# Optimization experiments

Measured on AMD Instinct MI355X. Metric: run time of the kernel, lower is better.

Reference implementation:

```python
import jax, jax.numpy as jnp
import numpy as np

jax.config.update("jax_enable_x64", True)  # faithful int64 hash arithmetic

N2_SIZES = [6619, 6637, 6653, 6659, 6661, 6673, 6679, 6689]
N3_SIZES = [65521, 65537, 65539, 65543, 65551, 65557, 65563, 65579]
SLOT_DIM = 80  # 1280 / (2 orders * 8 heads)
NUM_HEADS = 8
BATCH, SEQ = 8, 4096
VOCAB = 50257


def setup_inputs() -> dict:
    key = jax.random.key(0)
    ks = jax.random.split(key, 2 + 16)
    inp = {
        "canonical_ids": jax.random.randint(ks[0], (BATCH, SEQ), 0, VOCAB, dtype=jnp.int64),
        "hash_seeds": jax.random.randint(ks[1], (3, NUM_HEADS), 1, 2**31 - 1, dtype=jnp.int64),
    }
    i = 2
    for n, sizes in ((2, N2_SIZES), (3, N3_SIZES)):
        for h, sz in enumerate(sizes):
            inp[f"w_n{n}_h{h}"] = 0.02 * jax.random.normal(ks[i], (sz, SLOT_DIM), dtype=jnp.float32)
            i += 1
    return inp


def _ngrams(ids, n):
    # suffix n-grams per position, left-padded with 0: [B, S, n]
    padded = jnp.pad(ids, ((0, 0), (n - 1, 0)))
    S = ids.shape[1]
    return jnp.stack([padded[:, i:i + S] for i in range(n)], axis=-1)


def reference(canonical_ids, hash_seeds,
              w_n2_h0, w_n2_h1, w_n2_h2, w_n2_h3, w_n2_h4, w_n2_h5, w_n2_h6, w_n2_h7,
              w_n3_h0, w_n3_h1, w_n3_h2, w_n3_h3, w_n3_h4, w_n3_h5, w_n3_h6, w_n3_h7):
    tables = {
        2: [w_n2_h0, w_n2_h1, w_n2_h2, w_n2_h3, w_n2_h4, w_n2_h5, w_n2_h6, w_n2_h7],
        3: [w_n3_h0, w_n3_h1, w_n3_h2, w_n3_h3, w_n3_h4, w_n3_h5, w_n3_h6, w_n3_h7],
    }
    sizes = {2: N2_SIZES, 3: N3_SIZES}
    outs = []
    for n in (2, 3):
        ng = _ngrams(canonical_ids, n)                              # [B, S, n] int64
        seeds = hash_seeds[:n].T                                    # [H, n]
        terms = ng[:, :, None, :] * seeds[None, None, :, :]         # [B, S, H, n]
        h = terms[..., 0]
        for i in range(1, n):
            h = h ^ terms[..., i]                                   # [B, S, H]
        for k in range(NUM_HEADS):
            idx = h[:, :, k] % sizes[n][k]                          # [B, S]
            outs.append(tables[n][k][idx])                          # [B, S, SLOT_DIM]
    return jnp.concatenate(outs, axis=-1)                           # [B, S, 1280]
```

## Files before the change

### kernel.cpp

```cpp
#include <hip/hip_runtime.h>

typedef unsigned long long ull;
typedef float f4 __attribute__((ext_vector_type(4)));

__constant__ unsigned kSizes[16] = {
    6619u, 6637u, 6653u, 6659u, 6661u, 6673u, 6679u, 6689u,
    65521u, 65537u, 65539u, 65543u, 65551u, 65557u, 65563u, 65579u
};

__global__ __launch_bounds__(256)
void engram_idx_kernel(const int* __restrict__ ids,
                       const int* __restrict__ seeds,
                       int* __restrict__ idx_out)
{
    const int tid  = blockIdx.x * 256 + threadIdx.x;
    const int pos  = tid >> 4;
    const int slot = tid & 15;
    const int b = pos >> 12;
    const int s = pos & 4095;

    const int* row = ids + (b << 12);
    const int id0  = row[s];
    const int idm1 = (s >= 1) ? row[s - 1] : 0;

    const int head = slot & 7;
    const ull sa = (ull)(unsigned)seeds[head];
    const ull sb = (ull)(unsigned)seeds[8 + head];
    ull h;
    if (slot < 8) {
        h = ((ull)(unsigned)idm1 * sa) ^ ((ull)(unsigned)id0 * sb);
    } else {
        const int idm2 = (s >= 2) ? row[s - 2] : 0;
        const ull sc = (ull)(unsigned)seeds[16 + head];
        h = ((ull)(unsigned)idm2 * sa) ^ ((ull)(unsigned)idm1 * sb)
            ^ ((ull)(unsigned)id0 * sc);
    }
    idx_out[tid] = (int)(h % (ull)kSizes[slot]);
}

__global__ __launch_bounds__(320)
void engram_gather_kernel(const int* __restrict__ idx_in,
                          const float* __restrict__ t0,  const float* __restrict__ t1,
                          const float* __restrict__ t2,  const float* __restrict__ t3,
                          const float* __restrict__ t4,  const float* __restrict__ t5,
                          const float* __restrict__ t6,  const float* __restrict__ t7,
                          const float* __restrict__ t8,  const float* __restrict__ t9,
                          const float* __restrict__ t10, const float* __restrict__ t11,
                          const float* __restrict__ t12, const float* __restrict__ t13,
                          const float* __restrict__ t14, const float* __restrict__ t15,
                          f4* __restrict__ out)
{
    __shared__ const f4* tab[16];
    if (threadIdx.x == 0) {
        tab[0]=(const f4*)t0;   tab[1]=(const f4*)t1;   tab[2]=(const f4*)t2;   tab[3]=(const f4*)t3;
        tab[4]=(const f4*)t4;   tab[5]=(const f4*)t5;   tab[6]=(const f4*)t6;   tab[7]=(const f4*)t7;
        tab[8]=(const f4*)t8;   tab[9]=(const f4*)t9;   tab[10]=(const f4*)t10; tab[11]=(const f4*)t11;
        tab[12]=(const f4*)t12; tab[13]=(const f4*)t13; tab[14]=(const f4*)t14; tab[15]=(const f4*)t15;
    }
    __syncthreads();

    const int pos  = blockIdx.x;
    const int tx   = threadIdx.x;
    const int slot = tx / 20;
    const int off  = tx - slot * 20;

    const int ridx = idx_in[pos * 16 + slot];
    const f4  v    = tab[slot][ridx * 20 + off];

    __builtin_nontemporal_store(v, out + (size_t)pos * 320 + tx);
}

extern "C" void kernel_launch(void* const* d_in, const int* in_sizes, int n_in,
                              void* d_out, int out_size, void* d_ws, size_t ws_size,
                              hipStream_t stream) {
    const int* ids   = (const int*)d_in[0];
    const int* seeds = (const int*)d_in[1];
    const float* t[16];
    for (int i = 0; i < 16; ++i) t[i] = (const float*)d_in[2 + i];

    int* idx_buf = (int*)d_ws;

    engram_idx_kernel<<<dim3(2048), dim3(256), 0, stream>>>(ids, seeds, idx_buf);

    engram_gather_kernel<<<dim3(32768), dim3(320), 0, stream>>>(
        idx_buf,
        t[0], t[1], t[2], t[3], t[4], t[5], t[6], t[7],
        t[8], t[9], t[10], t[11], t[12], t[13], t[14], t[15],
        (f4*)d_out);
}
```

Baseline: 329.6 us.

## Fuse hash-index and gather kernels, replace 64-bit modulo with reciprocal multiply

Merges the index computation kernel into the gather kernel, so every output thread recomputes its n-gram hash and table row directly. This removes the intermediate index buffer round trip and one kernel launch. The 64-bit modulo is replaced by a double-precision reciprocal estimate of the quotient plus a one-step correction. In exchange, each thread redundantly loads ids and seeds and does 64-bit hash math (20 threads per slot), and the table pointer is now chosen from a per-thread array, which may cost registers or scratch memory.

```diff
diff --git a/kernel.cpp b/kernel.cpp
--- a/kernel.cpp
+++ b/kernel.cpp
@@ -7,67 +7,62 @@
     6619u, 6637u, 6653u, 6659u, 6661u, 6673u, 6679u, 6689u,
     65521u, 65537u, 65539u, 65543u, 65551u, 65557u, 65563u, 65579u
 };
+__constant__ double kInv[16] = {
+    1.0/6619.0,  1.0/6637.0,  1.0/6653.0,  1.0/6659.0,
+    1.0/6661.0,  1.0/6673.0,  1.0/6679.0,  1.0/6689.0,
+    1.0/65521.0, 1.0/65537.0, 1.0/65539.0, 1.0/65543.0,
+    1.0/65551.0, 1.0/65557.0, 1.0/65563.0, 1.0/65579.0
+};
 
 __global__ __launch_bounds__(256)
-void engram_idx_kernel(const int* __restrict__ ids,
-                       const int* __restrict__ seeds,
-                       int* __restrict__ idx_out)
+void engram_fused_kernel(const int* __restrict__ ids,
+                         const int* __restrict__ seeds,
+                         const float* __restrict__ t0,  const float* __restrict__ t1,
+                         const float* __restrict__ t2,  const float* __restrict__ t3,
+                         const float* __restrict__ t4,  const float* __restrict__ t5,
+                         const float* __restrict__ t6,  const float* __restrict__ t7,
+                         const float* __restrict__ t8,  const float* __restrict__ t9,
+                         const float* __restrict__ t10, const float* __restrict__ t11,
+                         const float* __restrict__ t12, const float* __restrict__ t13,
+                         const float* __restrict__ t14, const float* __restrict__ t15,
+                         f4* __restrict__ out)
 {
-    const int tid  = blockIdx.x * 256 + threadIdx.x;
-    const int pos  = tid >> 4;
-    const int slot = tid & 15;
+    const int tid = blockIdx.x * 256 + threadIdx.x;
+    const int pos = tid / 320;
+    const int tx  = tid - pos * 320;
+    const int slot = tx / 20;
+    const int off  = tx - slot * 20;
+
     const int b = pos >> 12;
     const int s = pos & 4095;
 
     const int* row = ids + (b << 12);
     const int id0  = row[s];
     const int idm1 = (s >= 1) ? row[s - 1] : 0;
+    const int idm2 = (s >= 2) ? row[s - 2] : 0;
 
     const int head = slot & 7;
     const ull sa = (ull)(unsigned)seeds[head];
     const ull sb = (ull)(unsigned)seeds[8 + head];
+    const ull sc = (ull)(unsigned)seeds[16 + head];
+
     ull h;
     if (slot < 8) {
         h = ((ull)(unsigned)idm1 * sa) ^ ((ull)(unsigned)id0 * sb);
     } else {
-        const int idm2 = (s >= 2) ? row[s - 2] : 0;
-        const ull sc = (ull)(unsigned)seeds[16 + head];
         h = ((ull)(unsigned)idm2 * sa) ^ ((ull)(unsigned)idm1 * sb)
             ^ ((ull)(unsigned)id0 * sc);
     }
-    idx_out[tid] = (int)(h % (ull)kSizes[slot]);
-}
+    const unsigned sz = kSizes[slot];
+    ull q = (ull)((double)h * kInv[slot]);
+    long long r = (long long)(h - q * (ull)sz);
+    if (r < 0)              r += sz;
+    else if (r >= (long long)sz) r -= sz;
+    const unsigned ridx = (unsigned)r;
 
-__global__ __launch_bounds__(320)
-void engram_gather_kernel(const int* __restrict__ idx_in,
-                          const float* __restrict__ t0,  const float* __restrict__ t1,
-                          const float* __restrict__ t2,  const float* __restrict__ t3,
-                          const float* __restrict__ t4,  const float* __restrict__ t5,
-                          const float* __restrict__ t6,  const float* __restrict__ t7,
-                          const float* __restrict__ t8,  const float* __restrict__ t9,
-                          const float* __restrict__ t10, const float* __restrict__ t11,
-                          const float* __restrict__ t12, const float* __restrict__ t13,
-                          const float* __restrict__ t14, const float* __restrict__ t15,
-                          f4* __restrict__ out)
-{
-    __shared__ const f4* tab[16];
-    if (threadIdx.x == 0) {
-        tab[0]=(const f4*)t0;   tab[1]=(const f4*)t1;   tab[2]=(const f4*)t2;   tab[3]=(const f4*)t3;
-        tab[4]=(const f4*)t4;   tab[5]=(const f4*)t5;   tab[6]=(const f4*)t6;   tab[7]=(const f4*)t7;
-        tab[8]=(const f4*)t8;   tab[9]=(const f4*)t9;   tab[10]=(const f4*)t10; tab[11]=(const f4*)t11;
-        tab[12]=(const f4*)t12; tab[13]=(const f4*)t13; tab[14]=(const f4*)t14; tab[15]=(const f4*)t15;
-    }
-    __syncthreads();
-
-    const int pos  = blockIdx.x;
-    const int tx   = threadIdx.x;
-    const int slot = tx / 20;
-    const int off  = tx - slot * 20;
-
-    const int ridx = idx_in[pos * 16 + slot];
-    const f4  v    = tab[slot][ridx * 20 + off];
-
-    __builtin_nontemporal_store(v, out + (size_t)pos * 320 + tx);
+    const float* tabs[16] = {t0,t1,t2,t3,t4,t5,t6,t7,t8,t9,t10,t11,t12,t13,t14,t15};
+    const f4* src = (const f4*)tabs[slot] + (size_t)ridx * 20 + off;
+    __builtin_nontemporal_store(*src, out + tid);
 }
 
 extern "C" void kernel_launch(void* const* d_in, const int* in_sizes, int n_in,
@@ -78,12 +73,8 @@
     const float* t[16];
     for (int i = 0; i < 16; ++i) t[i] = (const float*)d_in[2 + i];
 
-    int* idx_buf = (int*)d_ws;
-
-    engram_idx_kernel<<<dim3(2048), dim3(256), 0, stream>>>(ids, seeds, idx_buf);
-
-    engram_gather_kernel<<<dim3(32768), dim3(320), 0, stream>>>(
-        idx_buf,
+    engram_fused_kernel<<<dim3(40960), dim3(256), 0, stream>>>(
+        ids, seeds,
         t[0], t[1], t[2], t[3], t[4], t[5], t[6], t[7],
         t[8], t[9], t[10], t[11], t[12], t[13], t[14], t[15],
         (f4*)d_out);
```

Measured after the change: 340.9 us. 1.03x slower.
